# Performance work log

Measured on AMD Instinct MI355X. Metric: run time of the kernel, lower is better.

## Reference

```python
import jax, jax.numpy as jnp
import numpy as np

EPS = 1e-12  # matches torch F.normalize eps


def _l2n(x, axis):
    return x / jnp.maximum(jnp.linalg.norm(x, axis=axis, keepdims=True), EPS)


def setup_inputs() -> dict:
    key = jax.random.key(0)
    k1, k2, k3 = jax.random.split(key, 3)
    x = jax.random.normal(k1, (4, 128, 30, 40), dtype=jnp.float32)
    conv_w = jax.random.normal(k2, (64, 128), dtype=jnp.float32) * 0.02  # 1x1 conv, no bias (vladv2=False)
    centroids = jax.random.uniform(k3, (64, 128), dtype=jnp.float32)
    return {"x": x, "conv_w": conv_w, "centroids": centroids}


def reference(x, conv_w, centroids):
    N, C, H, W = x.shape
    K = centroids.shape[0]
    ps, stride = 4, 1  # patch_sizes='4', strides='1'

    # descriptor-wise L2 normalization of input
    x = _l2n(x, 1)

    # 1x1 conv + softmax over clusters -> soft assignment [N,K,H,W]
    soft_assign = jax.nn.softmax(jnp.einsum('kc,nchw->nkhw', conv_w, x), axis=1)

    # weighted residuals [N,K,C,H,W] (vectorized form of the per-cluster loop)
    res = (x[:, None] - centroids[None, :, :, None, None]) * soft_assign[:, :, None]

    # global VLAD: sum over spatial, intra-norm, flatten, L2-norm
    vlad_global = res.sum(axis=(-1, -2))            # [N,K,C]
    vlad_global = _l2n(vlad_global, 2).reshape(N, K * C)
    vlad_global = _l2n(vlad_global, 1)

    # integral image over spatial dims with zero pad on top/left
    r = res.reshape(N, K * C, H, W)
    integ = jnp.cumsum(jnp.cumsum(r, axis=-1), axis=-2)
    integ = jnp.pad(integ, ((0, 0), (0, 0), (1, 0), (1, 0)))  # [N,KC,H+1,W+1]

    # dilated 2x2 box-filter conv == 4-corner integral-image lookup
    TL = integ[:, :, :H + 1 - ps:stride, :W + 1 - ps:stride]
    TR = integ[:, :, :H + 1 - ps:stride, ps::stride]
    BL = integ[:, :, ps::stride, :W + 1 - ps:stride]
    BR = integ[:, :, ps::stride, ps::stride]
    vl = (TL - TR - BL + BR) / (ps * ps)            # [N,KC,Hp,Wp]
    Hp, Wp = vl.shape[-2], vl.shape[-1]

    # local VLAD: intra-norm over descriptor dim, then global L2 per patch
    vl = vl.reshape(N, K, C, Hp * Wp)
    vl = _l2n(vl, 2).reshape(N, K * C, Hp * Wp)
    vlad_local = _l2n(vl, 1)

    return vlad_global, vlad_local
```

## Files before the change

### kernel.cpp

```cpp
#include <hip/hip_runtime.h>
#include <math.h>

#define EPSV 1e-12f

namespace {
constexpr int N_  = 4;
constexpr int C_  = 128;
constexpr int H_  = 30;
constexpr int W_  = 40;
constexpr int K_  = 64;
constexpr int HW_ = H_ * W_;
constexpr int HP_ = 27;
constexpr int WP_ = 37;
constexpr int P_  = HP_ * WP_;
constexpr int PS_ = 1000;
constexpr int KC_ = K_ * C_;
constexpr int CP_ = C_ * P_;
constexpr int CS_ = HP_ * W_;
constexpr int SL_ = CS_ / 4;
constexpr int CVP_ = 132;
}

static __device__ __forceinline__ float4 ld4(const float* p) {
    return *reinterpret_cast<const float4*>(p);
}
static __device__ __forceinline__ float dot4(float4 a, float4 b) {
    return a.x * b.x + a.y * b.y + a.z * b.z + a.w * b.w;
}
static __device__ __forceinline__ float4 f4add(float4 a, float4 b) {
    return make_float4(a.x + b.x, a.y + b.y, a.z + b.z, a.w + b.w);
}
static __device__ __forceinline__ float4 f4mul(float4 a, float4 b) {
    return make_float4(a.x * b.x, a.y * b.y, a.z * b.z, a.w * b.w);
}

__global__ __launch_bounds__(256) void k1_norm_softmax(
    const float* __restrict__ x, const float* __restrict__ conv_w,
    float* __restrict__ xnT, float* __restrict__ xnP, float* __restrict__ sa)
{
    __shared__ float xrow[C_ * W_];
    __shared__ float conv_s[K_ * CVP_];
    __shared__ float xrowT[W_ * CVP_];
    __shared__ float invn[W_];
    __shared__ float s_s[K_ * W_];

    const int b = blockIdx.x;
    const int n = b / H_, h = b - n * H_;
    const int t = threadIdx.x;

    for (int i = t; i < C_ * W_; i += 256) {
        const int c = i / W_, w = i - c * W_;
        xrow[i] = x[(size_t)(n * C_ + c) * HW_ + h * W_ + w];
    }
    for (int i = t; i < K_ * C_; i += 256) {
        const int k = i >> 7, c = i & 127;
        conv_s[k * CVP_ + c] = conv_w[i];
    }
    __syncthreads();

    if (t < W_) {
        float s = 0.f;
        for (int c = 0; c < C_; ++c) { const float v = xrow[c * W_ + t]; s += v * v; }
        invn[t] = 1.f / fmaxf(sqrtf(s), EPSV);
    }
    __syncthreads();

    for (int i = t; i < C_ * W_; i += 256) {
        const int c = i / W_, w = i - c * W_;
        const float v = xrow[i] * invn[w];
        xrow[i] = v;
        xnT[(size_t)(n * C_ + c) * HW_ + h * W_ + w] = v;
    }
    __syncthreads();

    for (int i = t; i < W_ * C_; i += 256) {
        const int w = i / C_, c = i - w * C_;
        const float v = xrow[c * W_ + w];
        xnP[((size_t)n * HW_ + h * W_ + w) * C_ + c] = v;
        xrowT[w * CVP_ + c] = v;
    }
    __syncthreads();

    {
        const int k = t >> 2, q = t & 3;
        float acc0 = 0.f, acc1 = 0.f, acc2 = 0.f, acc3 = 0.f, acc4 = 0.f;
        float acc5 = 0.f, acc6 = 0.f, acc7 = 0.f, acc8 = 0.f, acc9 = 0.f;
        const float* convk = &conv_s[k * CVP_];
        for (int ch = 0; ch < 4; ++ch) {
            float4 cv0 = ld4(convk + ch * 32 + 0),  cv1 = ld4(convk + ch * 32 + 4);
            float4 cv2 = ld4(convk + ch * 32 + 8),  cv3 = ld4(convk + ch * 32 + 12);
            float4 cv4 = ld4(convk + ch * 32 + 16), cv5 = ld4(convk + ch * 32 + 20);
            float4 cv6 = ld4(convk + ch * 32 + 24), cv7 = ld4(convk + ch * 32 + 28);
#pragma unroll
            for (int wi = 0; wi < 10; ++wi) {
                const float* xw = &xrowT[(q * 10 + wi) * CVP_ + ch * 32];
                float s = dot4(cv0, ld4(xw)) + dot4(cv1, ld4(xw + 4))
                        + dot4(cv2, ld4(xw + 8)) + dot4(cv3, ld4(xw + 12))
                        + dot4(cv4, ld4(xw + 16)) + dot4(cv5, ld4(xw + 20))
                        + dot4(cv6, ld4(xw + 24)) + dot4(cv7, ld4(xw + 28));
                if      (wi == 0) acc0 += s; else if (wi == 1) acc1 += s;
                else if (wi == 2) acc2 += s; else if (wi == 3) acc3 += s;
                else if (wi == 4) acc4 += s; else if (wi == 5) acc5 += s;
                else if (wi == 6) acc6 += s; else if (wi == 7) acc7 += s;
                else if (wi == 8) acc8 += s; else              acc9 += s;
            }
        }
        float* sd = &s_s[k * W_ + q * 10];
        sd[0] = acc0; sd[1] = acc1; sd[2] = acc2; sd[3] = acc3; sd[4] = acc4;
        sd[5] = acc5; sd[6] = acc6; sd[7] = acc7; sd[8] = acc8; sd[9] = acc9;
    }
    __syncthreads();

    if (t < W_) {
        const int w = t;
        float m = -1e30f;
        for (int k = 0; k < K_; ++k) m = fmaxf(m, s_s[k * W_ + w]);
        float sum = 0.f;
        for (int k = 0; k < K_; ++k) sum += expf(s_s[k * W_ + w] - m);
        const float inv = 1.f / sum;
        for (int k = 0; k < K_; ++k)
            sa[(size_t)(n * K_ + k) * HW_ + h * W_ + w] = expf(s_s[k * W_ + w] - m) * inv;
    }
}

#define COLSUM_STRIP(cs_q, sa_s, xb, cA_base)                                   \
    if (t < 140) {                                                              \
        const int q2 = t / 70, item = t - q2 * 70;                              \
        const int hq = item / 10, wq = item - hq * 10;                          \
        const int h0 = 4 * hq;                                                  \
        const int nh = (hq < 6) ? 4 : 3;                                        \
        const int cA = (cA_base) + q2 * 16;                                     \
        const float* xp0 = xb + (size_t)(cA + 0)  * HW_ + h0 * W_ + 4 * wq;     \
        const float* xp1 = xb + (size_t)(cA + 4)  * HW_ + h0 * W_ + 4 * wq;     \
        const float* xp2 = xb + (size_t)(cA + 8)  * HW_ + h0 * W_ + 4 * wq;     \
        const float* xp3 = xb + (size_t)(cA + 12) * HW_ + h0 * W_ + 4 * wq;     \
        const float* sap = &sa_s[h0 * W_ + 4 * wq];                             \
        float4 p0[7], p1[7], p2[7], p3[7];                                      \
        _Pragma("unroll")                                                       \
        for (int r = 0; r < 7; ++r) {                                           \
            const float4 sv = ld4(sap + r * W_);                                \
            p0[r] = f4mul(sv, ld4(xp0 + r * W_));                               \
            p1[r] = f4mul(sv, ld4(xp1 + r * W_));                               \
            p2[r] = f4mul(sv, ld4(xp2 + r * W_));                               \
            p3[r] = f4mul(sv, ld4(xp3 + r * W_));                               \
        }                                                                       \
        _Pragma("unroll")                                                       \
        for (int hh = 0; hh < 4; ++hh) {                                        \
            if (hh < nh) {                                                      \
                const float4 c0v = f4add(f4add(p0[hh], p0[hh+1]), f4add(p0[hh+2], p0[hh+3])); \
                const float4 c1v = f4add(f4add(p1[hh], p1[hh+1]), f4add(p1[hh+2], p1[hh+3])); \
                const float4 c2v = f4add(f4add(p2[hh], p2[hh+1]), f4add(p2[hh+2], p2[hh+3])); \
                const float4 c3v = f4add(f4add(p3[hh], p3[hh+1]), f4add(p3[hh+2], p3[hh+3])); \
                const int s = 10 * (h0 + hh) + wq;                              \
                cs_q[q2][0][s] = make_float4(c0v.x, c1v.x, c2v.x, c3v.x);       \
                cs_q[q2][1][s] = make_float4(c0v.y, c1v.y, c2v.y, c3v.y);       \
                cs_q[q2][2][s] = make_float4(c0v.z, c1v.z, c2v.z, c3v.z);       \
                cs_q[q2][3][s] = make_float4(c0v.w, c1v.w, c2v.w, c3v.w);       \
            }                                                                   \
        }                                                                       \
    }

#define WINDOW10(csq, b0, d, A0, A1, A2, A3)                                    \
    {                                                                           \
        float4 v0 = csq[(b0 + 0) & 3][(b0 + 0) >> 2];                           \
        float4 v1 = csq[(b0 + 1) & 3][(b0 + 1) >> 2];                           \
        float4 v2 = csq[(b0 + 2) & 3][(b0 + 2) >> 2];                           \
        float4 v3 = csq[(b0 + 3) & 3][(b0 + 3) >> 2];                           \
        float4 v4 = csq[(b0 + 4) & 3][(b0 + 4) >> 2];                           \
        float4 v5 = csq[(b0 + 5) & 3][(b0 + 5) >> 2];                           \
        float4 v6 = csq[(b0 + 6) & 3][(b0 + 6) >> 2];                           \
        float4 v7 = csq[(b0 + 7) & 3][(b0 + 7) >> 2];                           \
        float4 v8 = csq[(b0 + 8) & 3][(b0 + 8) >> 2];                           \
        float4 v9 = csq[(b0 + 9) & 3][(b0 + 9) >> 2];                           \
        const float4 t0 = f4add(v0, v1), t1 = f4add(v1, v2), t2 = f4add(v2, v3);\
        const float4 t3 = f4add(v3, v4), t4 = f4add(v4, v5), t5 = f4add(v5, v6);\
        const float4 t6 = f4add(v6, v7), t7 = f4add(v7, v8), t8 = f4add(v8, v9);\
        const float4 w0 = f4add(t0, t2), w1 = f4add(t1, t3), w2 = f4add(t2, t4);\
        const float4 w3 = f4add(t3, t5), w4 = f4add(t4, t6), w5 = f4add(t5, t7);\
        const float4 w6 = f4add(t6, t8);                                        \
        A0 = (0 < d) ? w0 : w3;                                                 \
        A1 = (1 < d) ? w1 : w4;                                                 \
        A2 = (2 < d) ? w2 : w5;                                                 \
        A3 = (3 < d) ? w3 : w6;                                                 \
    }

__global__ __launch_bounds__(256) void k4_merged(
    const float* __restrict__ sa, const float* __restrict__ xnT,
    const float* __restrict__ xnP, const float* __restrict__ cent,
    float* __restrict__ nsqp, float* __restrict__ vg_u,
    float* __restrict__ vg_r)
{
    __shared__ float  sa_s[1248];
    __shared__ float4 cs_q[2][4][SL_ + 1];
    __shared__ float  gs[256], bss[256];
    __shared__ float  red[2];

    const int t = threadIdx.x;

    if (blockIdx.x < 256) {
        const int b = blockIdx.x;
        const int n = b >> 6, k = b & 63;
        const int c = t & 127, half = t >> 7;
        constexpr int HHW = HW_ / 2;

        const float* sarow = &sa[(size_t)b * HW_ + half * HHW];
        const float* xp = &xnP[((size_t)n * HW_ + half * HHW) * C_ + c];
        float g0 = 0.f, g1 = 0.f, g2 = 0.f, g3 = 0.f;
        float b0 = 0.f, b1 = 0.f, b2 = 0.f, b3 = 0.f;
        for (int pix = 0; pix < HHW; pix += 4) {
            const float s0 = sarow[pix + 0], s1 = sarow[pix + 1];
            const float s2 = sarow[pix + 2], s3 = sarow[pix + 3];
            g0 += s0 * xp[(size_t)(pix + 0) * C_];
            g1 += s1 * xp[(size_t)(pix + 1) * C_];
            g2 += s2 * xp[(size_t)(pix + 2) * C_];
            g3 += s3 * xp[(size_t)(pix + 3) * C_];
            b0 += s0; b1 += s1; b2 += s2; b3 += s3;
        }
        gs[t]  = (g0 + g1) + (g2 + g3);
        bss[t] = (b0 + b1) + (b2 + b3);
        __syncthreads();

        float vg = 0.f;
        if (t < 128) {
            vg = (gs[t] + gs[t + 128]) - cent[k * C_ + c] * (bss[t] + bss[t + 128]);
            float nsq = vg * vg;
            for (int off = 32; off >= 1; off >>= 1) nsq += __shfl_down(nsq, off);
            if ((t & 63) == 0) red[t >> 6] = nsq;
        }
        __syncthreads();
        const float tot  = red[0] + red[1];
        const float norm = sqrtf(tot);
        const float iv   = 1.f / fmaxf(norm, EPSV);
        if (t < 128) vg_u[(size_t)b * C_ + t] = vg * iv;
        if (t == 0) { const float rr = norm * iv; vg_r[b] = rr * rr; }
        return;
    }

    const int b  = blockIdx.x - 256;
    const int cq = b & 3;
    const int nk = b >> 2;
    const int n  = nk >> 6, k = nk & 63;

    for (int i = t; i < HW_; i += 256) sa_s[i] = sa[(size_t)nk * HW_ + i];
    __syncthreads();

    int b0 = 0, d = 4;
    float Bw0 = 0.f, Bw1 = 0.f, Bw2 = 0.f, Bw3 = 0.f;
    if (t < 250) {
        const int p0 = 4 * t;
        const int hp0 = p0 / WP_;
        const int wp0 = p0 - hp0 * WP_;
        b0 = p0 + 3 * hp0;
        d  = WP_ - wp0;
        const float* r0 = &sa_s[hp0 * W_ + wp0];
        float sc[10];
#pragma unroll
        for (int j = 0; j < 10; ++j)
            sc[j] = r0[j] + r0[j + W_] + r0[j + 2 * W_] + r0[j + 3 * W_];
        const float u0 = sc[0] + sc[1], u1 = sc[1] + sc[2], u2 = sc[2] + sc[3];
        const float u3 = sc[3] + sc[4], u4 = sc[4] + sc[5], u5 = sc[5] + sc[6];
        const float u6 = sc[6] + sc[7], u7 = sc[7] + sc[8], u8 = sc[8] + sc[9];
        const float wB0 = u0 + u2, wB1 = u1 + u3, wB2 = u2 + u4;
        const float wB3 = u3 + u5, wB4 = u4 + u6, wB5 = u5 + u7, wB6 = u6 + u8;
        Bw0 = (0 < d) ? wB0 : wB3;
        Bw1 = (1 < d) ? wB1 : wB4;
        Bw2 = (2 < d) ? wB2 : wB5;
        Bw3 = (3 < d) ? wB3 : wB6;
    }

    float nsq0 = 0.f, nsq1 = 0.f, nsq2 = 0.f, nsq3 = 0.f;
    const float* xb = xnT + (size_t)n * C_ * HW_;

    for (int iter = 0; iter < 4; ++iter) {
        const int c0 = cq * 32 + iter;
        __syncthreads();
        COLSUM_STRIP(cs_q, sa_s, xb, c0)
        __syncthreads();
        if (t < 250) {
            const float* ck = &cent[k * C_ + c0];
            const float4 ceA = make_float4(ck[0], ck[4], ck[8], ck[12]);
            const float4 ceB = make_float4(ck[16], ck[20], ck[24], ck[28]);
            float4 A0, A1, A2, A3, Q0, Q1, Q2, Q3;
            WINDOW10(cs_q[0], b0, d, A0, A1, A2, A3)
            WINDOW10(cs_q[1], b0, d, Q0, Q1, Q2, Q3)
            {
                const float4 e = make_float4(A0.x - ceA.x * Bw0, A0.y - ceA.y * Bw0,
                                             A0.z - ceA.z * Bw0, A0.w - ceA.w * Bw0);
                const float4 f = make_float4(Q0.x - ceB.x * Bw0, Q0.y - ceB.y * Bw0,
                                             Q0.z - ceB.z * Bw0, Q0.w - ceB.w * Bw0);
                nsq0 += dot4(e, e) + dot4(f, f);
            }
            {
                const float4 e = make_float4(A1.x - ceA.x * Bw1, A1.y - ceA.y * Bw1,
                                             A1.z - ceA.z * Bw1, A1.w - ceA.w * Bw1);
                const float4 f = make_float4(Q1.x - ceB.x * Bw1, Q1.y - ceB.y * Bw1,
                                             Q1.z - ceB.z * Bw1, Q1.w - ceB.w * Bw1);
                nsq1 += dot4(e, e) + dot4(f, f);
            }
            {
                const float4 e = make_float4(A2.x - ceA.x * Bw2, A2.y - ceA.y * Bw2,
                                             A2.z - ceA.z * Bw2, A2.w - ceA.w * Bw2);
                const float4 f = make_float4(Q2.x - ceB.x * Bw2, Q2.y - ceB.y * Bw2,
                                             Q2.z - ceB.z * Bw2, Q2.w - ceB.w * Bw2);
                nsq2 += dot4(e, e) + dot4(f, f);
            }
            {
                const float4 e = make_float4(A3.x - ceA.x * Bw3, A3.y - ceA.y * Bw3,
                                             A3.z - ceA.z * Bw3, A3.w - ceA.w * Bw3);
                const float4 f = make_float4(Q3.x - ceB.x * Bw3, Q3.y - ceB.y * Bw3,
                                             Q3.z - ceB.z * Bw3, Q3.w - ceB.w * Bw3);
                nsq3 += dot4(e, e) + dot4(f, f);
            }
        }
    }
    if (t < 250) {
        *reinterpret_cast<float4*>(&nsqp[(size_t)b * PS_ + 4 * t]) =
            make_float4(nsq0 * 0.00390625f, nsq1 * 0.00390625f,
                        nsq2 * 0.00390625f, nsq3 * 0.00390625f);
    }
}

__global__ __launch_bounds__(256) void k5_merged(
    const float* __restrict__ nsqp, float* __restrict__ inv1,
    float* __restrict__ rloc, const float* __restrict__ vg_u,
    const float* __restrict__ vg_r, float* __restrict__ out)
{
    const int t = threadIdx.x;
    if (blockIdx.x >= 256) {
        const int n = blockIdx.x - 256;
        __shared__ float inv2s;
        if (t == 0) {
            float s = 0.f;
            for (int k = 0; k < K_; ++k) s += vg_r[n * K_ + k];
            inv2s = 1.f / fmaxf(sqrtf(s), EPSV);
        }
        __syncthreads();
        const float inv2 = inv2s;
        for (int i = t; i < KC_; i += 256)
            out[(size_t)n * KC_ + i] = vg_u[(size_t)n * KC_ + i] * inv2;
        return;
    }
    const int nk = blockIdx.x;
    if (t < 250) {
        const int p0 = 4 * t;
        const float4 a = ld4(&nsqp[(size_t)(nk * 4 + 0) * PS_ + p0]);
        const float4 b = ld4(&nsqp[(size_t)(nk * 4 + 1) * PS_ + p0]);
        const float4 c = ld4(&nsqp[(size_t)(nk * 4 + 2) * PS_ + p0]);
        const float4 e = ld4(&nsqp[(size_t)(nk * 4 + 3) * PS_ + p0]);
        float4 iv, rr;
#pragma unroll
        for (int j = 0; j < 4; ++j) {
            const float s = reinterpret_cast<const float*>(&a)[j]
                          + reinterpret_cast<const float*>(&b)[j]
                          + reinterpret_cast<const float*>(&c)[j]
                          + reinterpret_cast<const float*>(&e)[j];
            const float norm = sqrtf(s);
            const float v = 1.f / fmaxf(norm, EPSV);
            reinterpret_cast<float*>(&iv)[j] = v * 0.0625f;
            const float r = norm * v;
            reinterpret_cast<float*>(&rr)[j] = r * r;
        }
        *reinterpret_cast<float4*>(&inv1[(size_t)nk * PS_ + p0]) = iv;
        *reinterpret_cast<float4*>(&rloc[(size_t)nk * PS_ + p0]) = rr;
    }
}

__global__ __launch_bounds__(256) void k6_inv2(
    const float* __restrict__ rloc, float* __restrict__ inv2)
{
    const int n = blockIdx.x;
    const int t = threadIdx.x;
    if (t < 250) {
        const int p0 = 4 * t;
        float4 s = make_float4(0, 0, 0, 0);
        for (int k = 0; k < K_; ++k) {
            const float4 r = ld4(&rloc[(size_t)(n * K_ + k) * PS_ + p0]);
            s = f4add(s, r);
        }
        float4 o;
        o.x = 1.f / fmaxf(sqrtf(s.x), EPSV);
        o.y = 1.f / fmaxf(sqrtf(s.y), EPSV);
        o.z = 1.f / fmaxf(sqrtf(s.z), EPSV);
        o.w = 1.f / fmaxf(sqrtf(s.w), EPSV);
        *reinterpret_cast<float4*>(&inv2[n * PS_ + p0]) = o;
    }
}

__global__ __launch_bounds__(256) void k7_write(
    const float* __restrict__ sa, const float* __restrict__ xnT,
    const float* __restrict__ cent, const float* __restrict__ inv1,
    const float* __restrict__ inv2, float* __restrict__ outl)
{
    __shared__ float  sa_s[1248];
    __shared__ float  scl_s[P_];
    __shared__ float  t2_s[P_];
    __shared__ float4 cs_q[2][4][SL_ + 1];

    const int b  = blockIdx.x;
    const int cq = b & 3;
    const int nk = b >> 2;
    const int n  = nk >> 6, k = nk & 63;
    const int t  = threadIdx.x;

    for (int i = t; i < HW_; i += 256) sa_s[i] = sa[(size_t)nk * HW_ + i];
    __syncthreads();
    for (int p = t; p < P_; p += 256) {
        const int hp = p / WP_, wp = p - hp * WP_;
        float bs = 0.f;
#pragma unroll
        for (int dh = 0; dh < 4; ++dh) {
            const float* r = &sa_s[(hp + dh) * W_ + wp];
            bs += r[0] + r[1] + r[2] + r[3];
        }
        const float sc = inv1[(size_t)nk * PS_ + p] * inv2[n * PS_ + p];
        scl_s[p] = sc;
        t2_s[p]  = bs * sc;
    }

    const float* xb = xnT + (size_t)n * C_ * HW_;
    float* ob = outl + (size_t)nk * CP_;

    for (int iter = 0; iter < 4; ++iter) {
        const int m = iter;
        const int c0 = cq * 32 + m;
        __syncthreads();
        COLSUM_STRIP(cs_q, sa_s, xb, c0)
        __syncthreads();
        const float* ck = &cent[k * C_ + c0];
        const float ce0 = ck[0],  ce1 = ck[4],  ce2 = ck[8],  ce3 = ck[12];
        const float ce4 = ck[16], ce5 = ck[20], ce6 = ck[24], ce7 = ck[28];
        float* ob0 = ob + (size_t)(c0 + 0)  * P_;
        float* ob1 = ob + (size_t)(c0 + 4)  * P_;
        float* ob2 = ob + (size_t)(c0 + 8)  * P_;
        float* ob3 = ob + (size_t)(c0 + 12) * P_;
        float* ob4 = ob + (size_t)(c0 + 16) * P_;
        float* ob5 = ob + (size_t)(c0 + 20) * P_;
        float* ob6 = ob + (size_t)(c0 + 24) * P_;
        float* ob7 = ob + (size_t)(c0 + 28) * P_;

        if (t < 249) {
            const int p0 = m + 4 * t;
            const int hp0 = p0 / WP_;
            const int wp0 = p0 - hp0 * WP_;
            const int b0 = p0 + 3 * hp0;
            const int d  = WP_ - wp0;
            const float sc0 = scl_s[p0 + 0], sc1 = scl_s[p0 + 1];
            const float sc2 = scl_s[p0 + 2], sc3 = scl_s[p0 + 3];
            const float tt0 = t2_s[p0 + 0], tt1 = t2_s[p0 + 1];
            const float tt2 = t2_s[p0 + 2], tt3 = t2_s[p0 + 3];
            float4 A0, A1, A2, A3, Q0, Q1, Q2, Q3;
            WINDOW10(cs_q[0], b0, d, A0, A1, A2, A3)
            WINDOW10(cs_q[1], b0, d, Q0, Q1, Q2, Q3)
            *reinterpret_cast<float4*>(ob0 + p0) =
                make_float4(A0.x * sc0 - ce0 * tt0, A1.x * sc1 - ce0 * tt1,
                            A2.x * sc2 - ce0 * tt2, A3.x * sc3 - ce0 * tt3);
            *reinterpret_cast<float4*>(ob1 + p0) =
                make_float4(A0.y * sc0 - ce1 * tt0, A1.y * sc1 - ce1 * tt1,
                            A2.y * sc2 - ce1 * tt2, A3.y * sc3 - ce1 * tt3);
            *reinterpret_cast<float4*>(ob2 + p0) =
                make_float4(A0.z * sc0 - ce2 * tt0, A1.z * sc1 - ce2 * tt1,
                            A2.z * sc2 - ce2 * tt2, A3.z * sc3 - ce2 * tt3);
            *reinterpret_cast<float4*>(ob3 + p0) =
                make_float4(A0.w * sc0 - ce3 * tt0, A1.w * sc1 - ce3 * tt1,
                            A2.w * sc2 - ce3 * tt2, A3.w * sc3 - ce3 * tt3);
            *reinterpret_cast<float4*>(ob4 + p0) =
                make_float4(Q0.x * sc0 - ce4 * tt0, Q1.x * sc1 - ce4 * tt1,
                            Q2.x * sc2 - ce4 * tt2, Q3.x * sc3 - ce4 * tt3);
            *reinterpret_cast<float4*>(ob5 + p0) =
                make_float4(Q0.y * sc0 - ce5 * tt0, Q1.y * sc1 - ce5 * tt1,
                            Q2.y * sc2 - ce5 * tt2, Q3.y * sc3 - ce5 * tt3);
            *reinterpret_cast<float4*>(ob6 + p0) =
                make_float4(Q0.z * sc0 - ce6 * tt0, Q1.z * sc1 - ce6 * tt1,
                            Q2.z * sc2 - ce6 * tt2, Q3.z * sc3 - ce6 * tt3);
            *reinterpret_cast<float4*>(ob7 + p0) =
                make_float4(Q0.w * sc0 - ce7 * tt0, Q1.w * sc1 - ce7 * tt1,
                            Q2.w * sc2 - ce7 * tt2, Q3.w * sc3 - ce7 * tt3);
        } else if (t < 252) {
            const int u = t - 249;
            const int p = (u < m) ? u : 996 + u;
            const int hp = p / WP_, wp = p - hp * WP_;
            const int base = hp * W_ + wp;
            const float4 a0 = cs_q[0][(base + 0) & 3][(base + 0) >> 2];
            const float4 a1 = cs_q[0][(base + 1) & 3][(base + 1) >> 2];
            const float4 a2 = cs_q[0][(base + 2) & 3][(base + 2) >> 2];
            const float4 a3 = cs_q[0][(base + 3) & 3][(base + 3) >> 2];
            const float4 q0 = cs_q[1][(base + 0) & 3][(base + 0) >> 2];
            const float4 q1 = cs_q[1][(base + 1) & 3][(base + 1) >> 2];
            const float4 q2 = cs_q[1][(base + 2) & 3][(base + 2) >> 2];
            const float4 q3 = cs_q[1][(base + 3) & 3][(base + 3) >> 2];
            const float sc = scl_s[p], tt = t2_s[p];
            ob0[p] = (a0.x + a1.x + a2.x + a3.x) * sc - ce0 * tt;
            ob1[p] = (a0.y + a1.y + a2.y + a3.y) * sc - ce1 * tt;
            ob2[p] = (a0.z + a1.z + a2.z + a3.z) * sc - ce2 * tt;
            ob3[p] = (a0.w + a1.w + a2.w + a3.w) * sc - ce3 * tt;
            ob4[p] = (q0.x + q1.x + q2.x + q3.x) * sc - ce4 * tt;
            ob5[p] = (q0.y + q1.y + q2.y + q3.y) * sc - ce5 * tt;
            ob6[p] = (q0.z + q1.z + q2.z + q3.z) * sc - ce6 * tt;
            ob7[p] = (q0.w + q1.w + q2.w + q3.w) * sc - ce7 * tt;
        }
    }
}

extern "C" void kernel_launch(void* const* d_in, const int* in_sizes, int n_in,
                              void* d_out, int out_size, void* d_ws, size_t ws_size,
                              hipStream_t stream)
{
    const float* x      = (const float*)d_in[0];
    const float* conv_w = (const float*)d_in[1];
    const float* cent   = (const float*)d_in[2];
    float* out = (float*)d_out;
    float* ws  = (float*)d_ws;

    float* xnT  = ws;
    float* xnP  = ws + 614400;
    float* sa   = ws + 1228800;
    float* vg_u = ws + 1536000;
    float* vg_r = ws + 1568768;
    float* nsqp = ws + 1569024;
    float* inv1 = ws + 2593024;
    float* rloc = ws + 2849024;
    float* inv2 = ws + 3105024;

    float* outl = out + (size_t)N_ * KC_;

    k1_norm_softmax<<<N_ * H_, 256, 0, stream>>>(x, conv_w, xnT, xnP, sa);
    k4_merged<<<256 + N_ * K_ * 4, 256, 0, stream>>>(sa, xnT, xnP, cent,
                                                     nsqp, vg_u, vg_r);
    k5_merged<<<256 + N_, 256, 0, stream>>>(nsqp, inv1, rloc, vg_u, vg_r, out);
    k6_inv2<<<N_, 256, 0, stream>>>(rloc, inv2);
    k7_write<<<N_ * K_ * 4, 256, 0, stream>>>(sa, xnT, cent, inv1, inv2, outl);
}
```

Baseline: 118.9 us.

## Split norm/softmax kernel across half-rows and parallelize reductions with shuffles

```diff
diff --git a/kernel.cpp b/kernel.cpp
--- a/kernel.cpp
+++ b/kernel.cpp
@@ -19,6 +19,7 @@
 constexpr int CS_ = HP_ * W_;
 constexpr int SL_ = CS_ / 4;
 constexpr int CVP_ = 132;
+constexpr int WH_ = 20;
 }
 
 static __device__ __forceinline__ float4 ld4(const float* p) {
@@ -38,19 +39,22 @@
     const float* __restrict__ x, const float* __restrict__ conv_w,
     float* __restrict__ xnT, float* __restrict__ xnP, float* __restrict__ sa)
 {
-    __shared__ float xrow[C_ * W_];
+    __shared__ float xrow[C_ * WH_];
     __shared__ float conv_s[K_ * CVP_];
-    __shared__ float xrowT[W_ * CVP_];
-    __shared__ float invn[W_];
-    __shared__ float s_s[K_ * W_];
-
-    const int b = blockIdx.x;
-    const int n = b / H_, h = b - n * H_;
+    __shared__ float xrowT[WH_ * CVP_];
+    __shared__ float invn[WH_];
+    __shared__ float s_s[K_ * WH_];
+
+    const int b  = blockIdx.x;
+    const int wh = b & 1;
+    const int nh = b >> 1;
+    const int n = nh / H_, h = nh - n * H_;
+    const int wbase = wh * WH_;
     const int t = threadIdx.x;
 
-    for (int i = t; i < C_ * W_; i += 256) {
-        const int c = i / W_, w = i - c * W_;
-        xrow[i] = x[(size_t)(n * C_ + c) * HW_ + h * W_ + w];
+    for (int i = t; i < C_ * WH_; i += 256) {
+        const int c = i / WH_, w = i - c * WH_;
+        xrow[i] = x[(size_t)(n * C_ + c) * HW_ + h * W_ + wbase + w];
     }
     for (int i = t; i < K_ * C_; i += 256) {
         const int k = i >> 7, c = i & 127;
@@ -58,33 +62,40 @@
     }
     __syncthreads();
 
-    if (t < W_) {
+    if (t < 8 * WH_) {
+        const int w = t >> 3, g = t & 7;
         float s = 0.f;
-        for (int c = 0; c < C_; ++c) { const float v = xrow[c * W_ + t]; s += v * v; }
-        invn[t] = 1.f / fmaxf(sqrtf(s), EPSV);
-    }
-    __syncthreads();
-
-    for (int i = t; i < C_ * W_; i += 256) {
-        const int c = i / W_, w = i - c * W_;
+#pragma unroll
+        for (int i = 0; i < 16; ++i) {
+            const float v = xrow[(g + 8 * i) * WH_ + w];
+            s += v * v;
+        }
+        s += __shfl_xor(s, 1);
+        s += __shfl_xor(s, 2);
+        s += __shfl_xor(s, 4);
+        if (g == 0) invn[w] = 1.f / fmaxf(sqrtf(s), EPSV);
+    }
+    __syncthreads();
+
+    for (int i = t; i < C_ * WH_; i += 256) {
+        const int c = i / WH_, w = i - c * WH_;
         const float v = xrow[i] * invn[w];
         xrow[i] = v;
-        xnT[(size_t)(n * C_ + c) * HW_ + h * W_ + w] = v;
-    }
-    __syncthreads();
-
-    for (int i = t; i < W_ * C_; i += 256) {
-        const int w = i / C_, c = i - w * C_;
-        const float v = xrow[c * W_ + w];
-        xnP[((size_t)n * HW_ + h * W_ + w) * C_ + c] = v;
+        xnT[(size_t)(n * C_ + c) * HW_ + h * W_ + wbase + w] = v;
+    }
+    __syncthreads();
+
+    for (int i = t; i < WH_ * C_; i += 256) {
+        const int w = i >> 7, c = i & 127;
+        const float v = xrow[c * WH_ + w];
+        xnP[((size_t)n * HW_ + h * W_ + wbase + w) * C_ + c] = v;
         xrowT[w * CVP_ + c] = v;
     }
     __syncthreads();
 
     {
-        const int k = t >> 2, q = t & 3;
-        float acc0 = 0.f, acc1 = 0.f, acc2 = 0.f, acc3 = 0.f, acc4 = 0.f;
-        float acc5 = 0.f, acc6 = 0.f, acc7 = 0.f, acc8 = 0.f, acc9 = 0.f;
+        const int k = t >> 2, wq = t & 3;
+        float acc[5] = {};
         const float* convk = &conv_s[k * CVP_];
         for (int ch = 0; ch < 4; ++ch) {
             float4 cv0 = ld4(convk + ch * 32 + 0),  cv1 = ld4(convk + ch * 32 + 4);
@@ -92,34 +103,41 @@
             float4 cv4 = ld4(convk + ch * 32 + 16), cv5 = ld4(convk + ch * 32 + 20);
             float4 cv6 = ld4(convk + ch * 32 + 24), cv7 = ld4(convk + ch * 32 + 28);
 #pragma unroll
-            for (int wi = 0; wi < 10; ++wi) {
-                const float* xw = &xrowT[(q * 10 + wi) * CVP_ + ch * 32];
-                float s = dot4(cv0, ld4(xw)) + dot4(cv1, ld4(xw + 4))
+            for (int j = 0; j < 5; ++j) {
+                const float* xw = &xrowT[(wq * 5 + j) * CVP_ + ch * 32];
+                acc[j] += dot4(cv0, ld4(xw)) + dot4(cv1, ld4(xw + 4))
                         + dot4(cv2, ld4(xw + 8)) + dot4(cv3, ld4(xw + 12))
                         + dot4(cv4, ld4(xw + 16)) + dot4(cv5, ld4(xw + 20))
                         + dot4(cv6, ld4(xw + 24)) + dot4(cv7, ld4(xw + 28));
-                if      (wi == 0) acc0 += s; else if (wi == 1) acc1 += s;
-                else if (wi == 2) acc2 += s; else if (wi == 3) acc3 += s;
-                else if (wi == 4) acc4 += s; else if (wi == 5) acc5 += s;
-                else if (wi == 6) acc6 += s; else if (wi == 7) acc7 += s;
-                else if (wi == 8) acc8 += s; else              acc9 += s;
             }
         }
-        float* sd = &s_s[k * W_ + q * 10];
-        sd[0] = acc0; sd[1] = acc1; sd[2] = acc2; sd[3] = acc3; sd[4] = acc4;
-        sd[5] = acc5; sd[6] = acc6; sd[7] = acc7; sd[8] = acc8; sd[9] = acc9;
-    }
-    __syncthreads();
-
-    if (t < W_) {
-        const int w = t;
-        float m = -1e30f;
-        for (int k = 0; k < K_; ++k) m = fmaxf(m, s_s[k * W_ + w]);
+        float* sd = &s_s[k * WH_ + wq * 5];
+#pragma unroll
+        for (int j = 0; j < 5; ++j) sd[j] = acc[j];
+    }
+    __syncthreads();
+
+    if (t < 8 * WH_) {
+        const int w = t >> 3, g = t & 7;
+        float sv[8];
+#pragma unroll
+        for (int kk = 0; kk < 8; ++kk) sv[kk] = s_s[(g + 8 * kk) * WH_ + w];
+        float m = fmaxf(fmaxf(fmaxf(sv[0], sv[1]), fmaxf(sv[2], sv[3])),
+                        fmaxf(fmaxf(sv[4], sv[5]), fmaxf(sv[6], sv[7])));
+        m = fmaxf(m, __shfl_xor(m, 1));
+        m = fmaxf(m, __shfl_xor(m, 2));
+        m = fmaxf(m, __shfl_xor(m, 4));
+        float ex[8];
         float sum = 0.f;
-        for (int k = 0; k < K_; ++k) sum += expf(s_s[k * W_ + w] - m);
+#pragma unroll
+        for (int kk = 0; kk < 8; ++kk) { ex[kk] = expf(sv[kk] - m); sum += ex[kk]; }
+        sum += __shfl_xor(sum, 1);
+        sum += __shfl_xor(sum, 2);
+        sum += __shfl_xor(sum, 4);
         const float inv = 1.f / sum;
-        for (int k = 0; k < K_; ++k)
-            sa[(size_t)(n * K_ + k) * HW_ + h * W_ + w] = expf(s_s[k * W_ + w] - m) * inv;
+#pragma unroll
+        for (int kk = 0; kk < 8; ++kk)
+            sa[(size_t)(n * K_ + g + 8 * kk) * HW_ + h * W_ + wbase + w] = ex[kk] * inv;
     }
 }
 
@@ -523,7 +541,7 @@
 
     float* outl = out + (size_t)N_ * KC_;
 
-    k1_norm_softmax<<<N_ * H_, 256, 0, stream>>>(x, conv_w, xnT, xnP, sa);
+    k1_norm_softmax<<<N_ * H_ * 2, 256, 0, stream>>>(x, conv_w, xnT, xnP, sa);
     k4_merged<<<256 + N_ * K_ * 4, 256, 0, stream>>>(sa, xnT, xnP, cent,
                                                      nsqp, vg_u, vg_r);
     k5_merged<<<256 + N_, 256, 0, stream>>>(nsqp, inv1, rloc, vg_u, vg_r, out);
```

New measurement: 110.8 us (median of 3 runs). -6.8%, faster.
